# Optimization experiments

Hardware: AMD Instinct MI355X
Metric: run time of the kernel (lower is better)

Reference implementation:

```python
import jax, jax.numpy as jnp
import numpy as np

EPS = 1e-5

def setup_inputs() -> dict:
    key = jax.random.key(0)
    ks = jax.random.split(key, 6)
    n, m, k, c_in, c_out = 200000, 50000, 16, 128, 256
    p = jax.random.normal(ks[0], (n, 3), dtype=jnp.float32)
    x = jax.random.normal(ks[1], (n, c_in), dtype=jnp.float32)
    o = jnp.sort(jax.random.randint(ks[2], (4,), 0, n)).astype(jnp.int64)
    n_p = jax.random.normal(ks[3], (m, 3), dtype=jnp.float32)
    knn_idx = jax.random.randint(ks[4], (m, k), 0, n).astype(jnp.int64)
    n_o = jnp.sort(jax.random.randint(ks[5], (4,), 0, m)).astype(jnp.int64)
    norm_w = jnp.ones((c_in,), dtype=jnp.float32)
    norm_b = jnp.zeros((c_in,), dtype=jnp.float32)
    W = jax.random.normal(jax.random.fold_in(key, 7), (c_out, c_in), dtype=jnp.float32) * (1.0 / np.sqrt(c_in))
    return {"p": p, "x": x, "o": o, "n_p": n_p, "knn_idx": knn_idx, "n_o": n_o,
            "norm_w": norm_w, "norm_b": norm_b, "W": W}

def reference(p, x, o, n_p, knn_idx, n_o, norm_w, norm_b, W):
    # Gather neighbor features: [m, k, c_in] (use_xyz=False so grouped_xyz is unused)
    feats = x[knn_idx]
    # LayerNorm over channel dim
    mu = jnp.mean(feats, axis=-1, keepdims=True)
    var = jnp.mean(jnp.square(feats - mu), axis=-1, keepdims=True)
    h = (feats - mu) * jax.lax.rsqrt(var + EPS) * norm_w + norm_b
    # Linear (no bias): torch Linear y = h @ W.T, W: [c_out, c_in]
    y = jnp.einsum('mkc,oc->mko', h, W)
    # MaxPool1d over the k neighbors
    out = jnp.max(y, axis=1)  # [m, c_out]
    return (out, n_p, n_o)
```

## Files before the change

### kernel.cpp

```cpp
#include <hip/hip_runtime.h>


#define C_IN   128
#define C_OUT  256
#define KNN    16
#define LN_EPS 1e-5f
#define BQ     2
#define ROWS   (BQ * KNN)
#define NBLK   1024

typedef __attribute__((ext_vector_type(8))) short  short8;
typedef __attribute__((ext_vector_type(4))) short  short4_t;
typedef __attribute__((ext_vector_type(8))) __bf16 bf16x8;
typedef __attribute__((ext_vector_type(4))) float  f32x4;

__device__ __forceinline__ short f2bf_bits(float f) {
    unsigned u = __float_as_uint(f);
    u += 0x7fffu + ((u >> 16) & 1u);
    return (short)(u >> 16);
}

__global__ __launch_bounds__(256) void fused_kernel(
    const float* __restrict__ x, const int* __restrict__ knn,
    const float* __restrict__ nw, const float* __restrict__ nb,
    const float* __restrict__ W,
    const float* __restrict__ n_p, const int* __restrict__ n_o,
    float* __restrict__ out, float* __restrict__ out_np, float* __restrict__ out_no,
    int mq, int npcnt)
{
    __shared__ __align__(16) short Ash[2 * ROWS * C_IN];

    const int tid  = threadIdx.x;
    const int lane = tid & 63;
    const int wave = tid >> 6;
    const int m16  = lane & 15;
    const int qd   = lane >> 4;

    short8 bfrag[4][4];
    float  cpart[4] = {0.f, 0.f, 0.f, 0.f};
    #pragma unroll
    for (int s = 0; s < 4; ++s) {
        const int k0 = s * 32 + qd * 8;
        const float4 a0 = *(const float4*)(nw + k0);
        const float4 a1 = *(const float4*)(nw + k0 + 4);
        const float4 c0 = *(const float4*)(nb + k0);
        const float4 c1 = *(const float4*)(nb + k0 + 4);
        const float nwv[8] = {a0.x,a0.y,a0.z,a0.w,a1.x,a1.y,a1.z,a1.w};
        const float nbv[8] = {c0.x,c0.y,c0.z,c0.w,c1.x,c1.y,c1.z,c1.w};
        #pragma unroll
        for (int t = 0; t < 4; ++t) {
            const int n = wave * 64 + t * 16 + m16;
            const float4* wp = (const float4*)(W + n * C_IN + k0);
            const float4 w0 = wp[0], w1 = wp[1];
            const float wvv[8] = {w0.x,w0.y,w0.z,w0.w,w1.x,w1.y,w1.z,w1.w};
            short8 b;
            #pragma unroll
            for (int j = 0; j < 8; ++j) {
                b[j] = f2bf_bits(wvv[j] * nwv[j]);
                cpart[t] += nbv[j] * wvv[j];
            }
            bfrag[t][s] = b;
        }
    }
    #pragma unroll
    for (int t = 0; t < 4; ++t) {
        cpart[t] += __shfl_xor(cpart[t], 16);
        cpart[t] += __shfl_xor(cpart[t], 32);
    }
    const float cbias = (qd == 0) ? cpart[0] : (qd == 1) ? cpart[1]
                      : (qd == 2) ? cpart[2] : cpart[3];

    const int sr = tid >> 3;
    const int sc = tid & 7;

    const int nbat = (mq + BQ - 1) / BQ;
    const int g = gridDim.x;

    int bat = blockIdx.x;
    float4 pf[4];
    int idxn;
    {
        const int id0 = knn[bat * ROWS + sr];
        const float* xr = x + (long long)id0 * C_IN + sc * 4;
        #pragma unroll
        for (int t = 0; t < 4; ++t) pf[t] = *(const float4*)(xr + t * 32);
        const int b1 = (bat + g < nbat) ? (bat + g) : bat;
        idxn = knn[b1 * ROWS + sr];
    }

    int buf = 0;
    for (; bat < nbat; bat += g) {
        float s1 = 0.f, s2 = 0.f;
        #pragma unroll
        for (int t = 0; t < 4; ++t) {
            s1 += pf[t].x + pf[t].y + pf[t].z + pf[t].w;
            s2 += pf[t].x*pf[t].x + pf[t].y*pf[t].y + pf[t].z*pf[t].z + pf[t].w*pf[t].w;
        }
        #pragma unroll
        for (int off = 1; off < 8; off <<= 1) {
            s1 += __shfl_xor(s1, off);
            s2 += __shfl_xor(s2, off);
        }
        const float mu   = s1 * (1.f / 128.f);
        const float rstd = rsqrtf(s2 * (1.f / 128.f) - mu * mu + LN_EPS);
        #pragma unroll
        for (int t = 0; t < 4; ++t) {
            short4_t hb;
            hb[0] = f2bf_bits((pf[t].x - mu) * rstd);
            hb[1] = f2bf_bits((pf[t].y - mu) * rstd);
            hb[2] = f2bf_bits((pf[t].z - mu) * rstd);
            hb[3] = f2bf_bits((pf[t].w - mu) * rstd);
            const int pb = ((sc >> 1) + 4 * t) ^ (sr & 15);
            *(short4_t*)&Ash[buf * 4096 + sr * 128 + pb * 8 + (sc & 1) * 4] = hb;
        }
        __syncthreads();

        if (bat + g < nbat) {
            const float* xr = x + (long long)idxn * C_IN + sc * 4;
            #pragma unroll
            for (int t = 0; t < 4; ++t) pf[t] = *(const float4*)(xr + t * 32);
            const int b2 = (bat + 2 * g < nbat) ? (bat + 2 * g) : (bat + g);
            idxn = knn[b2 * ROWS + sr];
        }

        #pragma unroll
        for (int ql = 0; ql < BQ; ++ql) {
            short8 afrag[4];
            #pragma unroll
            for (int s = 0; s < 4; ++s) {
                const int pb = (s * 4 + qd) ^ m16;
                afrag[s] = *(const short8*)&Ash[buf * 4096 + (ql * 16 + m16) * 128 + pb * 8];
            }
            f32x4 acc[4] = {{0,0,0,0},{0,0,0,0},{0,0,0,0},{0,0,0,0}};
            #pragma unroll
            for (int s = 0; s < 4; ++s) {
                const bf16x8 av = __builtin_bit_cast(bf16x8, afrag[s]);
                #pragma unroll
                for (int t = 0; t < 4; ++t)
                    acc[t] = __builtin_amdgcn_mfma_f32_16x16x32_bf16(
                        av, __builtin_bit_cast(bf16x8, bfrag[t][s]), acc[t], 0, 0, 0);
            }
            float r[4];
            #pragma unroll
            for (int t = 0; t < 4; ++t) {
                float v = fmaxf(fmaxf(acc[t][0], acc[t][1]), fmaxf(acc[t][2], acc[t][3]));
                v = fmaxf(v, __shfl_xor(v, 16));
                v = fmaxf(v, __shfl_xor(v, 32));
                r[t] = v;
            }
            const float vout = ((qd == 0) ? r[0] : (qd == 1) ? r[1]
                              : (qd == 2) ? r[2] : r[3]) + cbias;
            const int q = bat * BQ + ql;
            if (q < mq) out[q * C_OUT + wave * 64 + lane] = vout;
        }
        buf ^= 1;
    }

    const int gtid = blockIdx.x * 256 + tid;
    const int gstr = g * 256;
    const int np4 = npcnt >> 2;
    for (int i = gtid; i < np4; i += gstr)
        ((float4*)out_np)[i] = ((const float4*)n_p)[i];
    for (int i = (np4 << 2) + gtid; i < npcnt; i += gstr) out_np[i] = n_p[i];
    if (gtid < 4) out_no[gtid] = (float)n_o[gtid];
}

extern "C" void kernel_launch(void* const* d_in, const int* in_sizes, int n_in,
                              void* d_out, int out_size, void* d_ws, size_t ws_size,
                              hipStream_t stream)
{
    const float* x   = (const float*)d_in[1];
    const float* n_p = (const float*)d_in[3];
    const int*   knn = (const int*)  d_in[4];
    const int*   n_o = (const int*)  d_in[5];
    const float* nw  = (const float*)d_in[6];
    const float* nb  = (const float*)d_in[7];
    const float* W   = (const float*)d_in[8];
    float* out = (float*)d_out;

    const int mq    = in_sizes[4] / KNN;
    const int npcnt = in_sizes[3];
    float* out_np = out + (size_t)mq * C_OUT;
    float* out_no = out_np + npcnt;

    hipLaunchKernelGGL(fused_kernel, dim3(NBLK), dim3(256), 0, stream,
                       x, knn, nw, nb, W, n_p, n_o, out, out_np, out_no, mq, npcnt);
}
```

Measured before the change: 252.5 us.

## Stream gathered rows into LDS via global_load_lds and move LayerNorm to consumers

Gathered neighbour rows of x are now copied straight from global memory into a double-buffered fp32 LDS tile with global_load_lds, replacing the register prefetch. LayerNorm and the bf16 conversion move into the MFMA consumer loop, where each wave reads full fp32 rows from LDS and reduces mean and variance with shuffles. The aim is to free registers and let the hardware DMA overlap the irregular gathers with compute. In exchange, LDS use doubles, every wave recomputes the same LayerNorm statistics, and the unswizzled fp32 row reads may cause LDS bank conflicts.

```diff
diff --git a/kernel.cpp b/kernel.cpp
--- a/kernel.cpp
+++ b/kernel.cpp
@@ -7,10 +7,10 @@
 #define LN_EPS 1e-5f
 #define BQ     2
 #define ROWS   (BQ * KNN)
+#define TILE_F (ROWS * C_IN)
 #define NBLK   1024
 
 typedef __attribute__((ext_vector_type(8))) short  short8;
-typedef __attribute__((ext_vector_type(4))) short  short4_t;
 typedef __attribute__((ext_vector_type(8))) __bf16 bf16x8;
 typedef __attribute__((ext_vector_type(4))) float  f32x4;
 
@@ -18,6 +18,12 @@
     unsigned u = __float_as_uint(f);
     u += 0x7fffu + ((u >> 16) & 1u);
     return (short)(u >> 16);
+}
+
+__device__ __forceinline__ void dma16(const void* g, void* l) {
+    __builtin_amdgcn_global_load_lds(
+        (const __attribute__((address_space(1))) void*)g,
+        (__attribute__((address_space(3))) void*)l, 16, 0, 0);
 }
 
 __global__ __launch_bounds__(256) void fused_kernel(
@@ -28,13 +34,35 @@
     float* __restrict__ out, float* __restrict__ out_np, float* __restrict__ out_no,
     int mq, int npcnt)
 {
-    __shared__ __align__(16) short Ash[2 * ROWS * C_IN];
+    __shared__ __align__(16) float Ash[2 * TILE_F];
 
     const int tid  = threadIdx.x;
     const int lane = tid & 63;
     const int wave = tid >> 6;
     const int m16  = lane & 15;
     const int qd   = lane >> 4;
+    const int half = lane >> 5;
+    const int col  = lane & 31;
+
+    const int b0 = blockIdx.x;
+    const int g  = gridDim.x;
+    const int nbat = (mq + BQ - 1) / BQ;
+    const int maxflat = mq * KNN - 1;
+
+    int idxv[4];
+    if (b0 < nbat) {
+        #pragma unroll
+        for (int c = 0; c < 4; ++c) {
+            int flat = b0 * ROWS + wave * 8 + c * 2 + half;
+            flat = flat > maxflat ? maxflat : flat;
+            idxv[c] = knn[flat];
+        }
+        #pragma unroll
+        for (int c = 0; c < 4; ++c) {
+            const float* gp = x + (long long)idxv[c] * C_IN + col * 4;
+            dma16(gp, &Ash[(wave * 8 + c * 2) * C_IN]);
+        }
+    }
 
     short8 bfrag[4][4];
     float  cpart[4] = {0.f, 0.f, 0.f, 0.f};
@@ -70,83 +98,77 @@
     const float cbias = (qd == 0) ? cpart[0] : (qd == 1) ? cpart[1]
                       : (qd == 2) ? cpart[2] : cpart[3];
 
-    const int sr = tid >> 3;
-    const int sc = tid & 7;
-
-    const int nbat = (mq + BQ - 1) / BQ;
-    const int g = gridDim.x;
-
-    int bat = blockIdx.x;
-    float4 pf[4];
-    int idxn;
     {
-        const int id0 = knn[bat * ROWS + sr];
-        const float* xr = x + (long long)id0 * C_IN + sc * 4;
-        #pragma unroll
-        for (int t = 0; t < 4; ++t) pf[t] = *(const float4*)(xr + t * 32);
-        const int b1 = (bat + g < nbat) ? (bat + g) : bat;
-        idxn = knn[b1 * ROWS + sr];
+        int bn = b0 + g; if (bn >= nbat) bn = (nbat > 0) ? (nbat - 1) : 0;
+        #pragma unroll
+        for (int c = 0; c < 4; ++c) {
+            int flat = bn * ROWS + wave * 8 + c * 2 + half;
+            flat = flat > maxflat ? maxflat : flat;
+            idxv[c] = knn[flat];
+        }
     }
 
     int buf = 0;
-    for (; bat < nbat; bat += g) {
-        float s1 = 0.f, s2 = 0.f;
-        #pragma unroll
-        for (int t = 0; t < 4; ++t) {
-            s1 += pf[t].x + pf[t].y + pf[t].z + pf[t].w;
-            s2 += pf[t].x*pf[t].x + pf[t].y*pf[t].y + pf[t].z*pf[t].z + pf[t].w*pf[t].w;
-        }
-        #pragma unroll
-        for (int off = 1; off < 8; off <<= 1) {
-            s1 += __shfl_xor(s1, off);
-            s2 += __shfl_xor(s2, off);
-        }
-        const float mu   = s1 * (1.f / 128.f);
-        const float rstd = rsqrtf(s2 * (1.f / 128.f) - mu * mu + LN_EPS);
-        #pragma unroll
-        for (int t = 0; t < 4; ++t) {
-            short4_t hb;
-            hb[0] = f2bf_bits((pf[t].x - mu) * rstd);
-            hb[1] = f2bf_bits((pf[t].y - mu) * rstd);
-            hb[2] = f2bf_bits((pf[t].z - mu) * rstd);
-            hb[3] = f2bf_bits((pf[t].w - mu) * rstd);
-            const int pb = ((sc >> 1) + 4 * t) ^ (sr & 15);
-            *(short4_t*)&Ash[buf * 4096 + sr * 128 + pb * 8 + (sc & 1) * 4] = hb;
-        }
+    for (int bat = b0; bat < nbat; bat += g) {
         __syncthreads();
 
         if (bat + g < nbat) {
-            const float* xr = x + (long long)idxn * C_IN + sc * 4;
-            #pragma unroll
-            for (int t = 0; t < 4; ++t) pf[t] = *(const float4*)(xr + t * 32);
-            const int b2 = (bat + 2 * g < nbat) ? (bat + 2 * g) : (bat + g);
-            idxn = knn[b2 * ROWS + sr];
+            #pragma unroll
+            for (int c = 0; c < 4; ++c) {
+                const float* gp = x + (long long)idxv[c] * C_IN + col * 4;
+                dma16(gp, &Ash[(buf ^ 1) * TILE_F + (wave * 8 + c * 2) * C_IN]);
+            }
+        }
+        {
+            int bn = bat + 2 * g; if (bn >= nbat) bn = nbat - 1;
+            #pragma unroll
+            for (int c = 0; c < 4; ++c) {
+                int flat = bn * ROWS + wave * 8 + c * 2 + half;
+                flat = flat > maxflat ? maxflat : flat;
+                idxv[c] = knn[flat];
+            }
         }
 
         #pragma unroll
         for (int ql = 0; ql < BQ; ++ql) {
-            short8 afrag[4];
+            const float* tb = &Ash[buf * TILE_F + (ql * 16 + m16) * C_IN];
+            float v[32];
             #pragma unroll
             for (int s = 0; s < 4; ++s) {
-                const int pb = (s * 4 + qd) ^ m16;
-                afrag[s] = *(const short8*)&Ash[buf * 4096 + (ql * 16 + m16) * 128 + pb * 8];
-            }
+                const f32x4 a = *(const f32x4*)(tb + s * 32 + qd * 8);
+                const f32x4 b = *(const f32x4*)(tb + s * 32 + qd * 8 + 4);
+                v[s*8+0]=a[0]; v[s*8+1]=a[1]; v[s*8+2]=a[2]; v[s*8+3]=a[3];
+                v[s*8+4]=b[0]; v[s*8+5]=b[1]; v[s*8+6]=b[2]; v[s*8+7]=b[3];
+            }
+            float s1 = 0.f, s2 = 0.f;
+            #pragma unroll
+            for (int j = 0; j < 32; ++j) { s1 += v[j]; s2 += v[j] * v[j]; }
+            s1 += __shfl_xor(s1, 16); s1 += __shfl_xor(s1, 32);
+            s2 += __shfl_xor(s2, 16); s2 += __shfl_xor(s2, 32);
+            const float mu   = s1 * (1.f / 128.f);
+            const float rstd = rsqrtf(s2 * (1.f / 128.f) - mu * mu + LN_EPS);
+
             f32x4 acc[4] = {{0,0,0,0},{0,0,0,0},{0,0,0,0},{0,0,0,0}};
             #pragma unroll
             for (int s = 0; s < 4; ++s) {
-                const bf16x8 av = __builtin_bit_cast(bf16x8, afrag[s]);
+                short8 a;
+                #pragma unroll
+                for (int j = 0; j < 8; ++j)
+                    a[j] = f2bf_bits((v[s*8+j] - mu) * rstd);
+                const bf16x8 av = __builtin_bit_cast(bf16x8, a);
                 #pragma unroll
                 for (int t = 0; t < 4; ++t)
                     acc[t] = __builtin_amdgcn_mfma_f32_16x16x32_bf16(
                         av, __builtin_bit_cast(bf16x8, bfrag[t][s]), acc[t], 0, 0, 0);
             }
+
             float r[4];
             #pragma unroll
             for (int t = 0; t < 4; ++t) {
-                float v = fmaxf(fmaxf(acc[t][0], acc[t][1]), fmaxf(acc[t][2], acc[t][3]));
-                v = fmaxf(v, __shfl_xor(v, 16));
-                v = fmaxf(v, __shfl_xor(v, 32));
-                r[t] = v;
+                float vv = fmaxf(fmaxf(acc[t][0], acc[t][1]), fmaxf(acc[t][2], acc[t][3]));
+                vv = fmaxf(vv, __shfl_xor(vv, 16));
+                vv = fmaxf(vv, __shfl_xor(vv, 32));
+                r[t] = vv;
             }
             const float vout = ((qd == 0) ? r[0] : (qd == 1) ? r[1]
                               : (qd == 2) ? r[2] : r[3]) + cbias;
```

After: 357.2 us. 41.5% more time.
